# Kernel tuning notes

Hardware: AMD Instinct MI355X
Metric: run time of the kernel (lower is better)

The kernel has to match this reference:

```python
import jax, jax.numpy as jnp
import numpy as np

B, S, D, H = 2, 2048, 1024, 16
HD = D // H  # head_dim = 64


def setup_inputs() -> dict:
    key = jax.random.key(0)
    ks = jax.random.split(key, 12)
    s = 1.0 / np.sqrt(D)
    return {
        "query": jax.random.normal(ks[0], (B, S, D), jnp.float32),
        "key": jax.random.normal(ks[1], (B, S, D), jnp.float32),
        "value": jax.random.normal(ks[2], (B, S, D), jnp.float32),
        "attention_mask": jnp.zeros((B, S, S), jnp.float32),
        "WQ_w": jax.random.normal(ks[3], (D, D), jnp.float32) * s,
        "WQ_b": jnp.zeros((D,), jnp.float32),
        "WK_w": jax.random.normal(ks[4], (D, D), jnp.float32) * s,
        "WK_b": jnp.zeros((D,), jnp.float32),
        "WV_w": jax.random.normal(ks[5], (D, D), jnp.float32) * s,
        "WV_b": jnp.zeros((D,), jnp.float32),
        "WO_w": jax.random.normal(ks[6], (D, D), jnp.float32) * s,
        "WO_b": jnp.zeros((D,), jnp.float32),
    }


def _split_heads(x):
    # [B,S,D] -> [B,H,S,HD]
    b, s, _ = x.shape
    return x.reshape(b, s, H, HD).transpose(0, 2, 1, 3)


def reference(query, key, value, attention_mask,
              WQ_w, WQ_b, WK_w, WK_b, WV_w, WV_b, WO_w, WO_b):
    Q = _split_heads(query @ WQ_w.T + WQ_b)   # [B,H,S,HD]
    K = _split_heads(key @ WK_w.T + WK_b)
    V = _split_heads(value @ WV_w.T + WV_b)
    scale = 1.0 / jnp.sqrt(jnp.float32(HD))
    scores = jnp.einsum('bhqd,bhkd->bhqk', Q, K) * scale
    scores = scores + attention_mask[:, None, :, :]
    attn = jax.nn.softmax(scores, axis=-1)    # dropout_prob=0.0 -> identity
    out = jnp.einsum('bhqk,bhkd->bhqd', attn, V)
    out = out.transpose(0, 2, 1, 3).reshape(query.shape[0], -1, D)
    return out @ WO_w.T + WO_b
```

## Files before the change

kernel.cpp:

```cpp
#include <hip/hip_runtime.h>
#include <math.h>


typedef _Float16 h8 __attribute__((ext_vector_type(8)));
typedef _Float16 h4 __attribute__((ext_vector_type(4)));
typedef float f4 __attribute__((ext_vector_type(4)));

#define MFMA16(a, b, c) __builtin_amdgcn_mfma_f32_16x16x32_f16((a), (b), (c), 0, 0, 0)
#define EXP2F(x) __builtin_amdgcn_exp2f(x)

static constexpr int Bn = 2, Sn = 2048, Dn = 1024, Hn = 16, HDn = 64;
static constexpr int Mn = Bn * Sn;
static constexpr int Kn = Dn;
static constexpr int Nn = Dn;
static constexpr int LDP = 72;
static constexpr float LOG2E = 1.4426950408889634f;

__device__ __forceinline__ void gload_lds16(const _Float16* g, _Float16* l) {
  __builtin_amdgcn_global_load_lds(
      (const __attribute__((address_space(1))) unsigned int*)g,
      (__attribute__((address_space(3))) unsigned int*)l, 16, 0, 0);
}

struct CvtJobs {
  const float* src[7];
  _Float16* dst[7];
  int n4[7];
};

__global__ __launch_bounds__(256) void cvt_kernel(CvtJobs j) {
  const int stride = gridDim.x * blockDim.x;
  const int t0 = blockIdx.x * blockDim.x + threadIdx.x;
#pragma unroll
  for (int k = 0; k < 7; ++k) {
    const float4* __restrict__ s = (const float4*)j.src[k];
    h4* __restrict__ d = (h4*)j.dst[k];
    const int n = j.n4[k];
    for (int i = t0; i < n; i += stride) {
      const float4 f = s[i];
      h4 h;
      h[0] = (_Float16)f.x; h[1] = (_Float16)f.y;
      h[2] = (_Float16)f.z; h[3] = (_Float16)f.w;
      d[i] = h;
    }
  }
}

struct QkvArgs {
  const _Float16* X[3];
  const _Float16* W[3];
  const float* bias[3];
  _Float16* out[3];
};

__global__ __launch_bounds__(256) void gemm_qkv(QkvArgs args) {
  const int z = blockIdx.z;
  const _Float16* __restrict__ X = args.X[z];
  const _Float16* __restrict__ W = args.W[z];
  const float* __restrict__ bias = args.bias[z];
  _Float16* __restrict__ out = args.out[z];

  __shared__ _Float16 As[128 * 64];
  __shared__ _Float16 Bs[128 * 64];

  const int t = threadIdx.x;
  const int lane = t & 63, wv = t >> 6;
  const int l15 = lane & 15, quad = lane >> 4;
  const int wm = (wv >> 1) * 64, wn = (wv & 1) * 64;
  const int n0 = blockIdx.x * 128, m0 = blockIdx.y * 128;

  f4 acc[4][4];
#pragma unroll
  for (int i = 0; i < 4; ++i)
#pragma unroll
    for (int j = 0; j < 4; ++j) {
      f4 zz = {0.f, 0.f, 0.f, 0.f};
      acc[i][j] = zz;
    }

  const int srow = lane >> 3, scol = (lane & 7) * 8;

  for (int k0 = 0; k0 < Kn; k0 += 64) {
    __syncthreads();
#pragma unroll
    for (int u = 0; u < 4; ++u) {
      const int s = wv * 4 + u;
      const int row = s * 8 + srow;
      gload_lds16(X + (size_t)(m0 + row) * Kn + k0 + scol, As + s * 512);
      gload_lds16(W + (size_t)(n0 + row) * Kn + k0 + scol, Bs + s * 512);
    }
    __syncthreads();
#pragma unroll
    for (int kk = 0; kk < 64; kk += 32) {
      h8 af[4], bfr[4];
#pragma unroll
      for (int i = 0; i < 4; ++i)
        af[i] = *(const h8*)&As[(wm + i * 16 + l15) * 64 + kk + quad * 8];
#pragma unroll
      for (int j = 0; j < 4; ++j)
        bfr[j] = *(const h8*)&Bs[(wn + j * 16 + l15) * 64 + kk + quad * 8];
#pragma unroll
      for (int i = 0; i < 4; ++i)
#pragma unroll
        for (int j = 0; j < 4; ++j)
          acc[i][j] = MFMA16(af[i], bfr[j], acc[i][j]);
    }
  }

  const float osc = (z == 0) ? (0.125f * LOG2E) : 1.0f;
  if (z != 2) {
#pragma unroll
    for (int j = 0; j < 4; ++j) {
      const int n = n0 + wn + j * 16 + l15;
      const float bvs = bias[n] * osc;
      const int hh = n >> 6, hd = n & 63;
#pragma unroll
      for (int i = 0; i < 4; ++i) {
        const int mb = m0 + wm + i * 16 + quad * 4;
        const int bb = mb >> 11;
#pragma unroll
        for (int r = 0; r < 4; ++r) {
          const int ss = (mb + r) & (Sn - 1);
          out[(((size_t)(bb * Hn + hh)) * Sn + ss) * HDn + hd] =
              (_Float16)(acc[i][j][r] * osc + bvs);
        }
      }
    }
  } else {
#pragma unroll
    for (int j = 0; j < 4; ++j) {
      const int n = n0 + wn + j * 16 + l15;
      const float bv = bias[n];
      const int hh = n >> 6, hd = n & 63;
#pragma unroll
      for (int i = 0; i < 4; ++i) {
        const int mb = m0 + wm + i * 16 + quad * 4;
        const int bb = mb >> 11, ss = mb & (Sn - 1);
        h4 hv;
#pragma unroll
        for (int r = 0; r < 4; ++r) hv[r] = (_Float16)(acc[i][j][r] + bv);
        *(h4*)(out + (((size_t)(bb * Hn + hh)) * HDn + hd) * Sn + ss) = hv;
      }
    }
  }
}

__global__ __launch_bounds__(256) void gemm_o(const _Float16* __restrict__ X,
                                              const _Float16* __restrict__ W,
                                              const float* __restrict__ bias,
                                              float* __restrict__ out) {
  __shared__ _Float16 As[128 * 64];
  __shared__ _Float16 Bs[128 * 64];

  const int t = threadIdx.x;
  const int lane = t & 63, wv = t >> 6;
  const int l15 = lane & 15, quad = lane >> 4;
  const int wm = (wv >> 1) * 64, wn = (wv & 1) * 64;
  const int n0 = blockIdx.x * 128, m0 = blockIdx.y * 128;

  f4 acc[4][4];
#pragma unroll
  for (int i = 0; i < 4; ++i)
#pragma unroll
    for (int j = 0; j < 4; ++j) {
      f4 zz = {0.f, 0.f, 0.f, 0.f};
      acc[i][j] = zz;
    }

  const int srow = lane >> 3, scol = (lane & 7) * 8;

  for (int k0 = 0; k0 < Kn; k0 += 64) {
    __syncthreads();
#pragma unroll
    for (int u = 0; u < 4; ++u) {
      const int s = wv * 4 + u;
      const int row = s * 8 + srow;
      gload_lds16(X + (size_t)(m0 + row) * Kn + k0 + scol, As + s * 512);
      gload_lds16(W + (size_t)(n0 + row) * Kn + k0 + scol, Bs + s * 512);
    }
    __syncthreads();
#pragma unroll
    for (int kk = 0; kk < 64; kk += 32) {
      h8 af[4], bfr[4];
#pragma unroll
      for (int i = 0; i < 4; ++i)
        af[i] = *(const h8*)&As[(wm + i * 16 + l15) * 64 + kk + quad * 8];
#pragma unroll
      for (int j = 0; j < 4; ++j)
        bfr[j] = *(const h8*)&Bs[(wn + j * 16 + l15) * 64 + kk + quad * 8];
#pragma unroll
      for (int i = 0; i < 4; ++i)
#pragma unroll
        for (int j = 0; j < 4; ++j)
          acc[i][j] = MFMA16(af[i], bfr[j], acc[i][j]);
    }
  }

#pragma unroll
  for (int j = 0; j < 4; ++j) {
    const int n = n0 + wn + j * 16 + l15;
    const float bv = bias[n];
#pragma unroll
    for (int i = 0; i < 4; ++i) {
      const int mb = m0 + wm + i * 16 + quad * 4;
#pragma unroll
      for (int r = 0; r < 4; ++r)
        out[(size_t)(mb + r) * Nn + n] = acc[i][j][r] + bv;
    }
  }
}

__global__ __launch_bounds__(512) void attn_kernel(
    const _Float16* __restrict__ Qh,
    const _Float16* __restrict__ Kh,
    const _Float16* __restrict__ Vt,
    const float* __restrict__ mask,
    _Float16* __restrict__ out) {
  __shared__ _Float16 smem[4 * 64 * LDP];
  __shared__ _Float16 Pl[8 * 16 * LDP];

  const int t = threadIdx.x;
  const int w = t >> 6, lane = t & 63;
  const int l15 = lane & 15, quad = lane >> 4;
  const int g = w >> 2;
  const int wq = w & 3;

  const int bh = blockIdx.y;
  const int b = bh >> 4, h = bh & 15;
  const size_t headoff = (size_t)bh * Sn * HDn;
  const _Float16* Qp = Qh + headoff;
  const _Float16* Kp = Kh + headoff;
  const _Float16* Vp = Vt + headoff;

  const int qb = blockIdx.x * 64;
  const int q0 = qb + wq * 16;
  const h8 qf0 = *(const h8*)(Qp + (size_t)(q0 + l15) * HDn + quad * 8);
  const h8 qf1 = *(const h8*)(Qp + (size_t)(q0 + l15) * HDn + 32 + quad * 8);

  const int kbase = g * (Sn / 2);
  const float* mrow = mask + ((size_t)b * Sn + q0 + l15) * Sn + kbase;

  float m_run = -INFINITY, l_part = 0.f;
  f4 o_acc[4];
#pragma unroll
  for (int nt = 0; nt < 4; ++nt) {
    f4 zz = {0.f, 0.f, 0.f, 0.f};
    o_acc[nt] = zz;
  }

  _Float16* Kg = smem + g * (64 * LDP);
  _Float16* Vg = smem + (2 + g) * (64 * LDP);
  _Float16* Pw = &Pl[(w * 16) * LDP];

  const int tg = t & 255;
  const int srow = tg >> 3, sc8 = (tg & 7) * 8;
  const int srow1 = (tg + 256) >> 3, sc81 = ((tg + 256) & 7) * 8;

  constexpr int NT = (Sn / 2) / 64;

  uint4 kreg0, kreg1, vreg0, vreg1;
  float4 mreg[4];
  auto kv_issue = [&](int kt) {
    kreg0 = *(const uint4*)(Kp + (size_t)(kbase + kt * 64 + srow) * HDn + sc8);
    vreg0 = *(const uint4*)(Vp + (size_t)srow * Sn + kbase + kt * 64 + sc8);
    kreg1 = *(const uint4*)(Kp + (size_t)(kbase + kt * 64 + srow1) * HDn + sc81);
    vreg1 = *(const uint4*)(Vp + (size_t)srow1 * Sn + kbase + kt * 64 + sc81);
  };
  auto m_issue = [&](int kt) {
#pragma unroll
    for (int ks = 0; ks < 4; ++ks)
      mreg[ks] = *(const float4*)(mrow + kt * 64 + ks * 16 + quad * 4);
  };

  kv_issue(0);
  m_issue(0);

  for (int kt = 0; kt < NT; ++kt) {
    __syncthreads();
    *(uint4*)&Kg[srow * LDP + sc8] = kreg0;
    *(uint4*)&Vg[srow * LDP + sc8] = vreg0;
    *(uint4*)&Kg[srow1 * LDP + sc81] = kreg1;
    *(uint4*)&Vg[srow1 * LDP + sc81] = vreg1;
    __syncthreads();
    const int nx = (kt + 1 < NT) ? kt + 1 : kt;
    kv_issue(nx);

    f4 s[4];
#pragma unroll
    for (int ks = 0; ks < 4; ++ks) {
      const h8 kf0 = *(const h8*)&Kg[(ks * 16 + l15) * LDP + quad * 8];
      const h8 kf1 = *(const h8*)&Kg[(ks * 16 + l15) * LDP + 32 + quad * 8];
      f4 a = {0.f, 0.f, 0.f, 0.f};
      a = MFMA16(kf0, qf0, a);
      a = MFMA16(kf1, qf1, a);
#pragma unroll
      for (int r = 0; r < 4; ++r)
        s[ks][r] = fmaf(((const float*)&mreg[ks])[r], LOG2E, a[r]);
    }
    m_issue(nx);

    float mx = s[0][0];
#pragma unroll
    for (int ks = 0; ks < 4; ++ks)
#pragma unroll
      for (int r = 0; r < 4; ++r) mx = fmaxf(mx, s[ks][r]);
    mx = fmaxf(mx, __shfl_xor(mx, 16));
    mx = fmaxf(mx, __shfl_xor(mx, 32));
    const float nm = fmaxf(m_run, mx);
    const float alpha = EXP2F(m_run - nm);
    m_run = nm;
    float sm = 0.f;
#pragma unroll
    for (int ks = 0; ks < 4; ++ks)
#pragma unroll
      for (int r = 0; r < 4; ++r) {
        s[ks][r] = EXP2F(s[ks][r] - nm);
        sm += s[ks][r];
      }
    l_part = l_part * alpha + sm;
#pragma unroll
    for (int nt = 0; nt < 4; ++nt)
#pragma unroll
      for (int r = 0; r < 4; ++r) o_acc[nt][r] *= alpha;

#pragma unroll
    for (int ks = 0; ks < 4; ++ks) {
      h4 pv;
#pragma unroll
      for (int r = 0; r < 4; ++r) pv[r] = (_Float16)s[ks][r];
      *(h4*)&Pw[l15 * LDP + ks * 16 + quad * 4] = pv;
    }

#pragma unroll
    for (int kk = 0; kk < 64; kk += 32) {
      const h8 pf = *(const h8*)&Pw[l15 * LDP + kk + quad * 8];
#pragma unroll
      for (int nt = 0; nt < 4; ++nt) {
        const h8 vf = *(const h8*)&Vg[(nt * 16 + l15) * LDP + kk + quad * 8];
        o_acc[nt] = MFMA16(vf, pf, o_acc[nt]);
      }
    }
  }

  l_part += __shfl_xor(l_part, 16);
  l_part += __shfl_xor(l_part, 32);

  __syncthreads();
  float* Uex = (float*)smem;
  float* mex = Uex + 4 * 16 * LDP;
  float* lex = mex + 64;
  if (g == 1) {
#pragma unroll
    for (int nt = 0; nt < 4; ++nt)
      *(f4*)&Uex[wq * 16 * LDP + l15 * LDP + nt * 16 + quad * 4] = o_acc[nt];
    if (quad == 0) {
      mex[wq * 16 + l15] = m_run;
      lex[wq * 16 + l15] = l_part;
    }
  }
  __syncthreads();
  if (g == 0) {
    const float m1 = mex[wq * 16 + l15];
    const float l1 = lex[wq * 16 + l15];
    const float mm = fmaxf(m_run, m1);
    const float f0 = EXP2F(m_run - mm);
    const float f1 = EXP2F(m1 - mm);
    const float rl = 1.0f / (f0 * l_part + f1 * l1);
#pragma unroll
    for (int nt = 0; nt < 4; ++nt) {
      const f4 Ur = *(const f4*)&Uex[wq * 16 * LDP + l15 * LDP + nt * 16 + quad * 4];
      h4 ov;
#pragma unroll
      for (int r = 0; r < 4; ++r)
        ov[r] = (_Float16)((o_acc[nt][r] * f0 + Ur[r] * f1) * rl);
      *(h4*)&Pw[l15 * LDP + nt * 16 + quad * 4] = ov;
    }
    const int qr = lane >> 2;
    const int seg = (lane & 3) * 16;
    _Float16* dst = out + ((size_t)b * Sn + q0 + qr) * Dn + h * 64 + seg;
    *(uint4*)dst = *(const uint4*)&Pw[qr * LDP + seg];
    *(uint4*)(dst + 8) = *(const uint4*)&Pw[qr * LDP + seg + 8];
  }
}

extern "C" void kernel_launch(void* const* d_in, const int* in_sizes, int n_in,
                              void* d_out, int out_size, void* d_ws, size_t ws_size,
                              hipStream_t stream) {
  const float* q = (const float*)d_in[0];
  const float* k = (const float*)d_in[1];
  const float* v = (const float*)d_in[2];
  const float* mask = (const float*)d_in[3];
  const float* WQ = (const float*)d_in[4];
  const float* bQ = (const float*)d_in[5];
  const float* WK = (const float*)d_in[6];
  const float* bK = (const float*)d_in[7];
  const float* WV = (const float*)d_in[8];
  const float* bV = (const float*)d_in[9];
  const float* WO = (const float*)d_in[10];
  const float* bO = (const float*)d_in[11];

  _Float16* ws = (_Float16*)d_ws;
  const size_t MD = (size_t)Mn * Dn;
  const size_t DD = (size_t)Dn * Dn;
  _Float16* qh  = ws;
  _Float16* kh  = ws + MD;
  _Float16* vh  = ws + 2 * MD;
  _Float16* WQh = ws + 3 * MD;
  _Float16* WKh = WQh + DD;
  _Float16* WVh = WKh + DD;
  _Float16* WOh = WVh + DD;
  _Float16* Qh  = ws + 3 * MD + 4 * DD;
  _Float16* Kh  = Qh + MD;
  _Float16* Vt  = Kh + MD;
  _Float16* AO  = qh;

  CvtJobs cj;
  cj.src[0] = q;  cj.dst[0] = qh;  cj.n4[0] = (int)(MD / 4);
  cj.src[1] = k;  cj.dst[1] = kh;  cj.n4[1] = (int)(MD / 4);
  cj.src[2] = v;  cj.dst[2] = vh;  cj.n4[2] = (int)(MD / 4);
  cj.src[3] = WQ; cj.dst[3] = WQh; cj.n4[3] = (int)(DD / 4);
  cj.src[4] = WK; cj.dst[4] = WKh; cj.n4[4] = (int)(DD / 4);
  cj.src[5] = WV; cj.dst[5] = WVh; cj.n4[5] = (int)(DD / 4);
  cj.src[6] = WO; cj.dst[6] = WOh; cj.n4[6] = (int)(DD / 4);
  cvt_kernel<<<1024, 256, 0, stream>>>(cj);

  QkvArgs ga;
  ga.X[0] = qh; ga.W[0] = WQh; ga.bias[0] = bQ; ga.out[0] = Qh;
  ga.X[1] = kh; ga.W[1] = WKh; ga.bias[1] = bK; ga.out[1] = Kh;
  ga.X[2] = vh; ga.W[2] = WVh; ga.bias[2] = bV; ga.out[2] = Vt;
  gemm_qkv<<<dim3(Nn / 128, Mn / 128, 3), 256, 0, stream>>>(ga);

  attn_kernel<<<dim3(Sn / 64, Bn * Hn), 512, 0, stream>>>(Qh, Kh, Vt, mask, AO);

  gemm_o<<<dim3(Nn / 128, Mn / 128), 256, 0, stream>>>(AO, WOh, bO, (float*)d_out);
}
```

Measured before the change: 299.2 us.

## Process two 16-row query tiles per wave in attention to reuse K/V tiles

```diff
diff --git a/kernel.cpp b/kernel.cpp
--- a/kernel.cpp
+++ b/kernel.cpp
@@ -14,6 +14,7 @@
 static constexpr int Kn = Dn;
 static constexpr int Nn = Dn;
 static constexpr int LDP = 72;
+static constexpr int LDU = 68;
 static constexpr float LOG2E = 1.4426950408889634f;
 
 __device__ __forceinline__ void gload_lds16(const _Float16* g, _Float16* l) {
@@ -210,14 +211,14 @@
   }
 }
 
-__global__ __launch_bounds__(512) void attn_kernel(
+__global__ __launch_bounds__(512, 4) void attn_kernel(
     const _Float16* __restrict__ Qh,
     const _Float16* __restrict__ Kh,
     const _Float16* __restrict__ Vt,
     const float* __restrict__ mask,
     _Float16* __restrict__ out) {
   __shared__ _Float16 smem[4 * 64 * LDP];
-  __shared__ _Float16 Pl[8 * 16 * LDP];
+  __shared__ _Float16 Pl[8 * 32 * LDP];
 
   const int t = threadIdx.x;
   const int w = t >> 6, lane = t & 63;
@@ -232,25 +233,29 @@
   const _Float16* Kp = Kh + headoff;
   const _Float16* Vp = Vt + headoff;
 
-  const int qb = blockIdx.x * 64;
-  const int q0 = qb + wq * 16;
-  const h8 qf0 = *(const h8*)(Qp + (size_t)(q0 + l15) * HDn + quad * 8);
-  const h8 qf1 = *(const h8*)(Qp + (size_t)(q0 + l15) * HDn + 32 + quad * 8);
+  const int qb = blockIdx.x * 128;
+  const int q0 = qb + wq * 32;
+  const h8 qfA0 = *(const h8*)(Qp + (size_t)(q0 + l15) * HDn + quad * 8);
+  const h8 qfA1 = *(const h8*)(Qp + (size_t)(q0 + l15) * HDn + 32 + quad * 8);
+  const h8 qfB0 = *(const h8*)(Qp + (size_t)(q0 + 16 + l15) * HDn + quad * 8);
+  const h8 qfB1 = *(const h8*)(Qp + (size_t)(q0 + 16 + l15) * HDn + 32 + quad * 8);
 
   const int kbase = g * (Sn / 2);
-  const float* mrow = mask + ((size_t)b * Sn + q0 + l15) * Sn + kbase;
-
-  float m_run = -INFINITY, l_part = 0.f;
-  f4 o_acc[4];
+  const float* mrowA = mask + ((size_t)b * Sn + q0 + l15) * Sn + kbase;
+  const float* mrowB = mask + ((size_t)b * Sn + q0 + 16 + l15) * Sn + kbase;
+
+  float mA = -INFINITY, lA = 0.f, mB = -INFINITY, lB = 0.f;
+  f4 oA[4], oB[4];
 #pragma unroll
   for (int nt = 0; nt < 4; ++nt) {
     f4 zz = {0.f, 0.f, 0.f, 0.f};
-    o_acc[nt] = zz;
+    oA[nt] = zz;
+    oB[nt] = zz;
   }
 
   _Float16* Kg = smem + g * (64 * LDP);
   _Float16* Vg = smem + (2 + g) * (64 * LDP);
-  _Float16* Pw = &Pl[(w * 16) * LDP];
+  _Float16* Pw = &Pl[(w * 32) * LDP];
 
   const int tg = t & 255;
   const int srow = tg >> 3, sc8 = (tg & 7) * 8;
@@ -259,21 +264,14 @@
   constexpr int NT = (Sn / 2) / 64;
 
   uint4 kreg0, kreg1, vreg0, vreg1;
-  float4 mreg[4];
   auto kv_issue = [&](int kt) {
     kreg0 = *(const uint4*)(Kp + (size_t)(kbase + kt * 64 + srow) * HDn + sc8);
     vreg0 = *(const uint4*)(Vp + (size_t)srow * Sn + kbase + kt * 64 + sc8);
     kreg1 = *(const uint4*)(Kp + (size_t)(kbase + kt * 64 + srow1) * HDn + sc81);
     vreg1 = *(const uint4*)(Vp + (size_t)srow1 * Sn + kbase + kt * 64 + sc81);
   };
-  auto m_issue = [&](int kt) {
-#pragma unroll
-    for (int ks = 0; ks < 4; ++ks)
-      mreg[ks] = *(const float4*)(mrow + kt * 64 + ks * 16 + quad * 4);
-  };
 
   kv_issue(0);
-  m_issue(0);
 
   for (int kt = 0; kt < NT; ++kt) {
     __syncthreads();
@@ -285,101 +283,169 @@
     const int nx = (kt + 1 < NT) ? kt + 1 : kt;
     kv_issue(nx);
 
-    f4 s[4];
+    f4 sA[4], sB[4];
 #pragma unroll
     for (int ks = 0; ks < 4; ++ks) {
       const h8 kf0 = *(const h8*)&Kg[(ks * 16 + l15) * LDP + quad * 8];
       const h8 kf1 = *(const h8*)&Kg[(ks * 16 + l15) * LDP + 32 + quad * 8];
       f4 a = {0.f, 0.f, 0.f, 0.f};
-      a = MFMA16(kf0, qf0, a);
-      a = MFMA16(kf1, qf1, a);
-#pragma unroll
-      for (int r = 0; r < 4; ++r)
-        s[ks][r] = fmaf(((const float*)&mreg[ks])[r], LOG2E, a[r]);
-    }
-    m_issue(nx);
-
-    float mx = s[0][0];
-#pragma unroll
-    for (int ks = 0; ks < 4; ++ks)
-#pragma unroll
-      for (int r = 0; r < 4; ++r) mx = fmaxf(mx, s[ks][r]);
-    mx = fmaxf(mx, __shfl_xor(mx, 16));
-    mx = fmaxf(mx, __shfl_xor(mx, 32));
-    const float nm = fmaxf(m_run, mx);
-    const float alpha = EXP2F(m_run - nm);
-    m_run = nm;
-    float sm = 0.f;
-#pragma unroll
-    for (int ks = 0; ks < 4; ++ks)
+      a = MFMA16(kf0, qfA0, a);
+      a = MFMA16(kf1, qfA1, a);
+      f4 c = {0.f, 0.f, 0.f, 0.f};
+      c = MFMA16(kf0, qfB0, c);
+      c = MFMA16(kf1, qfB1, c);
+      const float4 mvA = *(const float4*)(mrowA + kt * 64 + ks * 16 + quad * 4);
+      const float4 mvB = *(const float4*)(mrowB + kt * 64 + ks * 16 + quad * 4);
 #pragma unroll
       for (int r = 0; r < 4; ++r) {
-        s[ks][r] = EXP2F(s[ks][r] - nm);
-        sm += s[ks][r];
-      }
-    l_part = l_part * alpha + sm;
-#pragma unroll
-    for (int nt = 0; nt < 4; ++nt)
-#pragma unroll
-      for (int r = 0; r < 4; ++r) o_acc[nt][r] *= alpha;
+        sA[ks][r] = fmaf(((const float*)&mvA)[r], LOG2E, a[r]);
+        sB[ks][r] = fmaf(((const float*)&mvB)[r], LOG2E, c[r]);
+      }
+    }
+
+    {
+      float mx = sA[0][0];
+#pragma unroll
+      for (int ks = 0; ks < 4; ++ks)
+#pragma unroll
+        for (int r = 0; r < 4; ++r) mx = fmaxf(mx, sA[ks][r]);
+      mx = fmaxf(mx, __shfl_xor(mx, 16));
+      mx = fmaxf(mx, __shfl_xor(mx, 32));
+      const float nm = fmaxf(mA, mx);
+      const float alpha = EXP2F(mA - nm);
+      mA = nm;
+      float sm = 0.f;
+#pragma unroll
+      for (int ks = 0; ks < 4; ++ks)
+#pragma unroll
+        for (int r = 0; r < 4; ++r) {
+          sA[ks][r] = EXP2F(sA[ks][r] - nm);
+          sm += sA[ks][r];
+        }
+      lA = lA * alpha + sm;
+#pragma unroll
+      for (int nt = 0; nt < 4; ++nt)
+#pragma unroll
+        for (int r = 0; r < 4; ++r) oA[nt][r] *= alpha;
+    }
+    {
+      float mx = sB[0][0];
+#pragma unroll
+      for (int ks = 0; ks < 4; ++ks)
+#pragma unroll
+        for (int r = 0; r < 4; ++r) mx = fmaxf(mx, sB[ks][r]);
+      mx = fmaxf(mx, __shfl_xor(mx, 16));
+      mx = fmaxf(mx, __shfl_xor(mx, 32));
+      const float nm = fmaxf(mB, mx);
+      const float alpha = EXP2F(mB - nm);
+      mB = nm;
+      float sm = 0.f;
+#pragma unroll
+      for (int ks = 0; ks < 4; ++ks)
+#pragma unroll
+        for (int r = 0; r < 4; ++r) {
+          sB[ks][r] = EXP2F(sB[ks][r] - nm);
+          sm += sB[ks][r];
+        }
+      lB = lB * alpha + sm;
+#pragma unroll
+      for (int nt = 0; nt < 4; ++nt)
+#pragma unroll
+        for (int r = 0; r < 4; ++r) oB[nt][r] *= alpha;
+    }
 
 #pragma unroll
     for (int ks = 0; ks < 4; ++ks) {
-      h4 pv;
-#pragma unroll
-      for (int r = 0; r < 4; ++r) pv[r] = (_Float16)s[ks][r];
-      *(h4*)&Pw[l15 * LDP + ks * 16 + quad * 4] = pv;
-    }
-
-#pragma unroll
-    for (int kk = 0; kk < 64; kk += 32) {
-      const h8 pf = *(const h8*)&Pw[l15 * LDP + kk + quad * 8];
+      h4 pa, pb;
+#pragma unroll
+      for (int r = 0; r < 4; ++r) {
+        pa[r] = (_Float16)sA[ks][r];
+        pb[r] = (_Float16)sB[ks][r];
+      }
+      *(h4*)&Pw[l15 * LDP + ks * 16 + quad * 4] = pa;
+      *(h4*)&Pw[(16 + l15) * LDP + ks * 16 + quad * 4] = pb;
+    }
+
+#pragma unroll
+    for (int j = 0; j < 2; ++j) {
+      const h8 pfA = *(const h8*)&Pw[l15 * LDP + j * 32 + quad * 8];
+      const h8 pfB = *(const h8*)&Pw[(16 + l15) * LDP + j * 32 + quad * 8];
 #pragma unroll
       for (int nt = 0; nt < 4; ++nt) {
-        const h8 vf = *(const h8*)&Vg[(nt * 16 + l15) * LDP + kk + quad * 8];
-        o_acc[nt] = MFMA16(vf, pf, o_acc[nt]);
-      }
-    }
-  }
-
-  l_part += __shfl_xor(l_part, 16);
-  l_part += __shfl_xor(l_part, 32);
+        const h8 vf = *(const h8*)&Vg[(nt * 16 + l15) * LDP + j * 32 + quad * 8];
+        oA[nt] = MFMA16(vf, pfA, oA[nt]);
+        oB[nt] = MFMA16(vf, pfB, oB[nt]);
+      }
+    }
+  }
+
+  lA += __shfl_xor(lA, 16);
+  lA += __shfl_xor(lA, 32);
+  lB += __shfl_xor(lB, 16);
+  lB += __shfl_xor(lB, 32);
 
   __syncthreads();
   float* Uex = (float*)smem;
-  float* mex = Uex + 4 * 16 * LDP;
-  float* lex = mex + 64;
+  float* mex = Uex + 4 * 32 * LDU;
+  float* lex = mex + 128;
   if (g == 1) {
 #pragma unroll
-    for (int nt = 0; nt < 4; ++nt)
-      *(f4*)&Uex[wq * 16 * LDP + l15 * LDP + nt * 16 + quad * 4] = o_acc[nt];
+    for (int nt = 0; nt < 4; ++nt) {
+      *(f4*)&Uex[(wq * 32 + l15) * LDU + nt * 16 + quad * 4] = oA[nt];
+      *(f4*)&Uex[(wq * 32 + 16 + l15) * LDU + nt * 16 + quad * 4] = oB[nt];
+    }
     if (quad == 0) {
-      mex[wq * 16 + l15] = m_run;
-      lex[wq * 16 + l15] = l_part;
+      mex[wq * 32 + l15] = mA;
+      lex[wq * 32 + l15] = lA;
+      mex[wq * 32 + 16 + l15] = mB;
+      lex[wq * 32 + 16 + l15] = lB;
     }
   }
   __syncthreads();
   if (g == 0) {
-    const float m1 = mex[wq * 16 + l15];
-    const float l1 = lex[wq * 16 + l15];
-    const float mm = fmaxf(m_run, m1);
-    const float f0 = EXP2F(m_run - mm);
-    const float f1 = EXP2F(m1 - mm);
-    const float rl = 1.0f / (f0 * l_part + f1 * l1);
-#pragma unroll
-    for (int nt = 0; nt < 4; ++nt) {
-      const f4 Ur = *(const f4*)&Uex[wq * 16 * LDP + l15 * LDP + nt * 16 + quad * 4];
-      h4 ov;
-#pragma unroll
-      for (int r = 0; r < 4; ++r)
-        ov[r] = (_Float16)((o_acc[nt][r] * f0 + Ur[r] * f1) * rl);
-      *(h4*)&Pw[l15 * LDP + nt * 16 + quad * 4] = ov;
-    }
-    const int qr = lane >> 2;
-    const int seg = (lane & 3) * 16;
+    {
+      const float m1 = mex[wq * 32 + l15];
+      const float l1 = lex[wq * 32 + l15];
+      const float mm = fmaxf(mA, m1);
+      const float f0 = EXP2F(mA - mm);
+      const float f1 = EXP2F(m1 - mm);
+      const float rl = 1.0f / (f0 * lA + f1 * l1);
+#pragma unroll
+      for (int nt = 0; nt < 4; ++nt) {
+        const f4 Ur = *(const f4*)&Uex[(wq * 32 + l15) * LDU + nt * 16 + quad * 4];
+        h4 ov;
+#pragma unroll
+        for (int r = 0; r < 4; ++r)
+          ov[r] = (_Float16)((oA[nt][r] * f0 + Ur[r] * f1) * rl);
+        *(h4*)&Pw[l15 * LDP + nt * 16 + quad * 4] = ov;
+      }
+    }
+    {
+      const float m1 = mex[wq * 32 + 16 + l15];
+      const float l1 = lex[wq * 32 + 16 + l15];
+      const float mm = fmaxf(mB, m1);
+      const float f0 = EXP2F(mB - mm);
+      const float f1 = EXP2F(m1 - mm);
+      const float rl = 1.0f / (f0 * lB + f1 * l1);
+#pragma unroll
+      for (int nt = 0; nt < 4; ++nt) {
+        const f4 Ur =
+            *(const f4*)&Uex[(wq * 32 + 16 + l15) * LDU + nt * 16 + quad * 4];
+        h4 ov;
+#pragma unroll
+        for (int r = 0; r < 4; ++r)
+          ov[r] = (_Float16)((oB[nt][r] * f0 + Ur[r] * f1) * rl);
+        *(h4*)&Pw[(16 + l15) * LDP + nt * 16 + quad * 4] = ov;
+      }
+    }
+    const int qr = lane >> 1;
+    const int seg = (lane & 1) * 32;
     _Float16* dst = out + ((size_t)b * Sn + q0 + qr) * Dn + h * 64 + seg;
-    *(uint4*)dst = *(const uint4*)&Pw[qr * LDP + seg];
-    *(uint4*)(dst + 8) = *(const uint4*)&Pw[qr * LDP + seg + 8];
+    const _Float16* srcp = &Pw[qr * LDP + seg];
+    *(uint4*)dst = *(const uint4*)srcp;
+    *(uint4*)(dst + 8) = *(const uint4*)(srcp + 8);
+    *(uint4*)(dst + 16) = *(const uint4*)(srcp + 16);
+    *(uint4*)(dst + 24) = *(const uint4*)(srcp + 24);
   }
 }
 
@@ -430,7 +496,7 @@
   ga.X[2] = vh; ga.W[2] = WVh; ga.bias[2] = bV; ga.out[2] = Vt;
   gemm_qkv<<<dim3(Nn / 128, Mn / 128, 3), 256, 0, stream>>>(ga);
 
-  attn_kernel<<<dim3(Sn / 64, Bn * Hn), 512, 0, stream>>>(Qh, Kh, Vt, mask, AO);
+  attn_kernel<<<dim3(Sn / 128, Bn * Hn), 512, 0, stream>>>(Qh, Kh, Vt, mask, AO);
 
   gemm_o<<<dim3(Nn / 128, Mn / 128), 256, 0, stream>>>(AO, WOh, bO, (float*)d_out);
 }
```

New measurement: 326.8 us. +9.2%, slower.
